# Kernel tuning notes

Hardware: AMD Instinct MI355X
Metric: run time of the kernel (lower is better)

The kernel has to match this reference:

```python
import jax, jax.numpy as jnp
import numpy as np

TOP_K = 2
HORIZON = 10


def _lstm_layer(seq, w_ih, w_hh, b_ih, b_hh):
    """Single torch-style LSTM layer over seq [T, in]; returns hidden seq [T, hid]."""
    hid = w_hh.shape[1]
    def step(carry, x_t):
        h, c = carry
        z = x_t @ w_ih.T + h @ w_hh.T + b_ih + b_hh  # [4*hid], torch gate order i,f,g,o
        i, f, g, o = jnp.split(z, 4)
        c = jax.nn.sigmoid(f) * c + jax.nn.sigmoid(i) * jnp.tanh(g)
        h = jax.nn.sigmoid(o) * jnp.tanh(c)
        return (h, c), h
    init = (jnp.zeros((hid,), seq.dtype), jnp.zeros((hid,), seq.dtype))
    _, hs = jax.lax.scan(step, init, seq)
    return hs


def setup_inputs() -> dict:
    key = jax.random.key(0)
    ks = jax.random.split(key, 12)
    H, E = 4096, 64
    B, S = 4, 4096
    s = 0.02
    return {
        "x": jax.random.normal(ks[0], (B, S, H), jnp.float32),
        "gate_w": jax.random.normal(ks[1], (E, H), jnp.float32) * s,
        "expert_bias": jnp.zeros((E,), jnp.float32),
        "cp_w1": jax.random.normal(ks[2], (64, H), jnp.float32) * s,
        "cp_b1": jnp.zeros((64,), jnp.float32),
        "cp_w2": jax.random.normal(ks[3], (1, 64), jnp.float32) * s,
        "cp_b2": jnp.zeros((1,), jnp.float32),
        "load_buffer": jax.random.uniform(ks[4], (50, E), jnp.float32),
        "lp_w_ih0": jax.random.normal(ks[5], (256, E), jnp.float32) * s,
        "lp_w_hh0": jax.random.normal(ks[6], (256, 64), jnp.float32) * s,
        "lp_b_ih0": jnp.zeros((256,), jnp.float32),
        "lp_b_hh0": jnp.zeros((256,), jnp.float32),
        "lp_w_ih1": jax.random.normal(ks[7], (256, 64), jnp.float32) * s,
        "lp_w_hh1": jax.random.normal(ks[8], (256, 64), jnp.float32) * s,
        "lp_b_ih1": jnp.zeros((256,), jnp.float32),
        "lp_b_hh1": jnp.zeros((256,), jnp.float32),
        "head_w": jax.random.normal(ks[9], (E * HORIZON, 64), jnp.float32) * s,
        "head_b": jnp.zeros((E * HORIZON,), jnp.float32),
    }


def reference(x, gate_w, expert_bias, cp_w1, cp_b1, cp_w2, cp_b2, load_buffer,
              lp_w_ih0, lp_w_hh0, lp_b_ih0, lp_b_hh0,
              lp_w_ih1, lp_w_hh1, lp_b_ih1, lp_b_hh1, head_w, head_b):
    sg = jax.lax.stop_gradient
    B, S, H = x.shape
    E = gate_w.shape[0]
    flat = x.reshape(-1, H)                       # [N, H]
    N = flat.shape[0]

    # --- routing logits (small gate GEMM) ---
    logits = flat @ gate_w.T                      # [N, E]

    # --- LSTM load prediction (torch.no_grad in original) ---
    seq = sg(load_buffer)
    h1 = _lstm_layer(seq, sg(lp_w_ih0), sg(lp_w_hh0), sg(lp_b_ih0), sg(lp_b_hh0))
    h2 = _lstm_layer(h1, sg(lp_w_ih1), sg(lp_w_hh1), sg(lp_b_ih1), sg(lp_b_hh1))
    pred = h2[-1] @ sg(head_w).T + sg(head_b)     # [E*HORIZON]
    future_load = jax.nn.softmax(pred.reshape(E, HORIZON).mean(axis=1))  # [E]

    # --- bias + predicted-load adjustment, softmax, top-k ---
    adj_logits = logits + expert_bias - sg(future_load)
    probs = jax.nn.softmax(adj_logits, axis=-1)   # [N, E]
    top_scores, top_idx = jax.lax.top_k(probs, TOP_K)
    top_scores = top_scores / top_scores.sum(axis=-1, keepdims=True)

    # --- switch-style load-balancing auxiliary loss ---
    one_hot = jax.nn.one_hot(top_idx, E, dtype=probs.dtype)   # [N, k, E]
    f = one_hot.sum(axis=(0, 1)) / (N * TOP_K)                # routed fraction per expert
    P = probs.mean(axis=0)                                    # mean routing prob
    aux_loss = E * jnp.sum(f * P)

    # --- dynamic capacity from complexity predictor (torch.no_grad) ---
    comp = jax.nn.sigmoid(
        jax.nn.relu(flat @ sg(cp_w1).T + sg(cp_b1)) @ sg(cp_w2).T + sg(cp_b2))  # [N,1]
    capacity = jnp.clip(0.5 + 1.5 * comp.mean(), 0.5, 2.0)

    return top_scores, top_idx, aux_loss, capacity, future_load
```

## Files before the change

### kernel.cpp

```cpp
#include <hip/hip_runtime.h>
#include <stdint.h>

#define IMG_OFF_BYTES 80000
#define CHUNK_IMG 16384
#define LOGITS_OFF 680000
#define TAU 1e-3f

#define XLOFF 5120
#define BUF_STRIDE 10240

typedef __attribute__((ext_vector_type(8))) short short8v;
typedef __attribute__((ext_vector_type(4))) short short4v;
typedef __attribute__((ext_vector_type(4))) float f32x4;

__device__ __forceinline__ float rlf(float v, int l) {
  return __int_as_float(__builtin_amdgcn_readlane(__float_as_int(v), l));
}
__device__ __forceinline__ float wsum(float v) {
#pragma unroll
  for (int o = 32; o; o >>= 1) v += __shfl_xor(v, o, 64);
  return v;
}
__device__ __forceinline__ float wmax(float v) {
#pragma unroll
  for (int o = 32; o; o >>= 1) v = fmaxf(v, __shfl_xor(v, o, 64));
  return v;
}
__device__ __forceinline__ unsigned short f2bf(float f) {
  unsigned u = __float_as_uint(f);
  u += 0x7fffu + ((u >> 16) & 1u);
  return (unsigned short)(u >> 16);
}
__device__ __forceinline__ float bf2f(unsigned short h) {
  return __uint_as_float(((unsigned)h) << 16);
}
__device__ __forceinline__ short8v frag8(const char* p0, const char* p1) {
  short4v a = *(const short4v*)p0;
  short4v b = *(const short4v*)p1;
  return __builtin_shufflevector(a, b, 0, 1, 2, 3, 4, 5, 6, 7);
}

__global__ __launch_bounds__(256) void prep_kernel(
    const float* __restrict__ gate_w, const float* __restrict__ cp_w1,
    float* __restrict__ ws)
{
  const int c = blockIdx.x;
  const int tid = threadIdx.x;
  if (c == 0 && tid < 144) ws[64 + tid] = 0.f;
  {
    float4 z = make_float4(0.f, 0.f, 0.f, 0.f);
    float4* lz = (float4*)(ws + LOGITS_OFF + c * 16384);
#pragma unroll
    for (int i = 0; i < 16; ++i) lz[tid + i * 256] = z;
  }
  const int row = tid >> 1;
  const int half = tid & 1;
  const float* src = ((row < 64) ? (gate_w + (size_t)row * 4096)
                                 : (cp_w1 + (size_t)(row - 64) * 4096)) + c * 32 + half * 16;
  float v[16];
#pragma unroll
  for (int j = 0; j < 4; ++j) *(float4*)&v[j * 4] = *(const float4*)(src + j * 4);
  const int g = row >> 4, r15 = row & 15;
  char* img = (char*)ws + IMG_OFF_BYTES + (size_t)c * CHUNK_IMG + g * 2048;
#pragma unroll
  for (int q = 0; q < 4; ++q) {
    unsigned short h0 = f2bf(v[4 * q + 0]), h1 = f2bf(v[4 * q + 1]);
    unsigned short h2 = f2bf(v[4 * q + 2]), h3 = f2bf(v[4 * q + 3]);
    unsigned short l0 = f2bf(v[4 * q + 0] - bf2f(h0));
    unsigned short l1 = f2bf(v[4 * q + 1] - bf2f(h1));
    unsigned short l2 = f2bf(v[4 * q + 2] - bf2f(h2));
    unsigned short l3 = f2bf(v[4 * q + 3] - bf2f(h3));
    uint2 hv, lv;
    hv.x = (unsigned)h0 | ((unsigned)h1 << 16);
    hv.y = (unsigned)h2 | ((unsigned)h3 << 16);
    lv.x = (unsigned)l0 | ((unsigned)l1 << 16);
    lv.y = (unsigned)l2 | ((unsigned)l3 << 16);
    const int l = q * 16 + r15;
    *(uint2*)(img + l * 16 + half * 8) = hv;
    *(uint2*)(img + 1024 + l * 16 + half * 8) = lv;
  }
}

__device__ void lstm_device(
    char* ldsbase,
    const float* __restrict__ lb,
    const float* __restrict__ wih0, const float* __restrict__ whh0,
    const float* __restrict__ bih0, const float* __restrict__ bhh0,
    const float* __restrict__ wih1, const float* __restrict__ whh1,
    const float* __restrict__ bih1, const float* __restrict__ bhh1,
    const float* __restrict__ head_w, const float* __restrict__ head_b,
    float* __restrict__ ws, float* __restrict__ out, int N)
{
  float* seqh = (float*)ldsbase;
  float* h1s  = seqh + 3200;
  float* zbuf = h1s + 3200;
  float* hbuf = zbuf + 256;
  float* preds = hbuf + 64;
  const int tid = threadIdx.x;
  const int lane = tid & 63;
  for (int i = tid; i < 3200; i += 256) seqh[i] = lb[i];

  float hv = 0.f;
#pragma unroll 1
  for (int L = 0; L < 2; ++L) {
    const float* wip  = L ? wih1 : wih0;
    const float* whp  = L ? whh1 : whh0;
    const float* bip  = L ? bih1 : bih0;
    const float* bhp  = L ? bhh1 : bhh0;
    const float* seqp = L ? h1s  : seqh;
    float wiR[64], whR[64];
#pragma unroll
    for (int j = 0; j < 64; j += 4) {
      *(float4*)&wiR[j] = *(const float4*)(wip + tid * 64 + j);
      *(float4*)&whR[j] = *(const float4*)(whp + tid * 64 + j);
    }
    const float bsum = bip[tid] + bhp[tid];
    float c_reg = 0.f;
    hv = 0.f;
    if (tid < 64) hbuf[tid] = 0.f;
    __syncthreads();
#pragma unroll 1
    for (int t = 0; t < 50; ++t) {
      const float xv = seqp[t * 64 + lane];
      float a0 = bsum, a1 = 0.f, a2 = 0.f, a3 = 0.f;
#pragma unroll
      for (int j = 0; j < 64; j += 4) {
        a0 = fmaf(rlf(xv, j + 0), wiR[j + 0], a0);
        a1 = fmaf(rlf(xv, j + 1), wiR[j + 1], a1);
        a2 = fmaf(rlf(xv, j + 2), wiR[j + 2], a2);
        a3 = fmaf(rlf(xv, j + 3), wiR[j + 3], a3);
      }
#pragma unroll
      for (int j = 0; j < 64; j += 4) {
        a0 = fmaf(rlf(hv, j + 0), whR[j + 0], a0);
        a1 = fmaf(rlf(hv, j + 1), whR[j + 1], a1);
        a2 = fmaf(rlf(hv, j + 2), whR[j + 2], a2);
        a3 = fmaf(rlf(hv, j + 3), whR[j + 3], a3);
      }
      zbuf[tid] = (a0 + a1) + (a2 + a3);
      __syncthreads();
      if (tid < 64) {
        const float zi = zbuf[tid], zf = zbuf[64 + tid];
        const float zg = zbuf[128 + tid], zo = zbuf[192 + tid];
        const float si = 1.f / (1.f + expf(-zi));
        const float sf = 1.f / (1.f + expf(-zf));
        const float so = 1.f / (1.f + expf(-zo));
        c_reg = sf * c_reg + si * tanhf(zg);
        const float h = so * tanhf(c_reg);
        hbuf[tid] = h;
        if (L == 0) h1s[t * 64 + tid] = h;
      }
      __syncthreads();
      hv = hbuf[lane];
    }
    __syncthreads();
  }
  for (int o = tid; o < 640; o += 256) {
    const float* hw = head_w + o * 64;
    float a0 = 0.f, a1 = 0.f, a2 = 0.f, a3 = 0.f;
#pragma unroll
    for (int j = 0; j < 64; j += 4) {
      a0 = fmaf(rlf(hv, j + 0), hw[j + 0], a0);
      a1 = fmaf(rlf(hv, j + 1), hw[j + 1], a1);
      a2 = fmaf(rlf(hv, j + 2), hw[j + 2], a2);
      a3 = fmaf(rlf(hv, j + 3), hw[j + 3], a3);
    }
    preds[o] = (a0 + a1) + (a2 + a3) + head_b[o];
  }
  __syncthreads();
  if (tid < 64) {
    float m = 0.f;
#pragma unroll
    for (int h = 0; h < 10; ++h) m += preds[tid * 10 + h];
    m = m / 10.f;
    const float mx = wmax(m);
    const float p = expf(m - mx);
    const float s = wsum(p);
    const float flv = p / s;
    ws[tid] = flv;
    out[4 * N + 2 + tid] = flv;
  }
}

__global__ __launch_bounds__(256, 1) void gemm_kernel(
    const float* __restrict__ x, float* __restrict__ ws, float* __restrict__ out,
    const float* __restrict__ lb,
    const float* __restrict__ wih0, const float* __restrict__ whh0,
    const float* __restrict__ bih0, const float* __restrict__ bhh0,
    const float* __restrict__ wih1, const float* __restrict__ whh1,
    const float* __restrict__ bih1, const float* __restrict__ bhh1,
    const float* __restrict__ head_w, const float* __restrict__ head_b,
    int N)
{
  __shared__ __align__(16) char lds[30720];
  if (blockIdx.x == 0) {
    lstm_device(lds, lb, wih0, whh0, bih0, bhh0, wih1, whh1, bih1, bhh1,
                head_w, head_b, ws, out, N);
    return;
  }
  const int b = blockIdx.x - 1;
  const int tb = (b & 255) * 64;
  const int ck0 = (b >> 8) * 32;
  const int tid = threadIdx.x;
  const int lane = tid & 63;
  const int wv = __builtin_amdgcn_readfirstlane(tid >> 6);
  const int r15 = lane & 15;
  const int fo = (lane >> 4) * 8;
  const int row = tid >> 2;
  const int kslot = tid & 3;
  const float* xsrc = x + (size_t)(tb + row) * 4096 + kslot * 8;
  const char* wimg = (const char*)ws + IMG_OFF_BYTES;
  char* buf0 = lds;
  char* buf1 = lds + BUF_STRIDE;

  f32x4 acc[4][2];
#pragma unroll
  for (int mi = 0; mi < 4; ++mi)
#pragma unroll
    for (int ni = 0; ni < 2; ++ni) acc[mi][ni] = (f32x4)0.f;

  float xa[8], xb[8];
  short8v wh[2], wl[2];

#define LOADX(R, C)                                                        \
  { *(float4*)&R[0] = *(const float4*)(xsrc + (size_t)(C) * 32);           \
    *(float4*)&R[4] = *(const float4*)(xsrc + (size_t)(C) * 32 + 4); }

#define WRITEX(R, BASE)                                                    \
  { uint4 hv, lv; unsigned hu[4], lu[4];                                   \
    _Pragma("unroll")                                                      \
    for (int i = 0; i < 4; ++i) {                                          \
      unsigned short h0 = f2bf(R[2 * i]), h1 = f2bf(R[2 * i + 1]);         \
      unsigned short l0 = f2bf(R[2 * i] - bf2f(h0));                       \
      unsigned short l1 = f2bf(R[2 * i + 1] - bf2f(h1));                   \
      hu[i] = (unsigned)h0 | ((unsigned)h1 << 16);                         \
      lu[i] = (unsigned)l0 | ((unsigned)l1 << 16);                         \
    }                                                                      \
    hv.x = hu[0]; hv.y = hu[1]; hv.z = hu[2]; hv.w = hu[3];                \
    lv.x = lu[0]; lv.y = lu[1]; lv.z = lu[2]; lv.w = lu[3];                \
    *(uint4*)((BASE) + row * 80 + kslot * 16) = hv;                        \
    *(uint4*)((BASE) + XLOFF + row * 80 + kslot * 16) = lv; }

#define WLOAD(C)                                                           \
  { const char* wb = wimg + (size_t)(C) * CHUNK_IMG + wv * 4096 + lane * 16; \
    wh[0] = *(const short8v*)wb;                                           \
    wl[0] = *(const short8v*)(wb + 1024);                                  \
    wh[1] = *(const short8v*)(wb + 2048);                                  \
    wl[1] = *(const short8v*)(wb + 3072); }

#define COMPUTE(BASE)                                                      \
  { short8v xh[4], xl[4];                                                  \
    _Pragma("unroll")                                                      \
    for (int mi = 0; mi < 4; ++mi) {                                       \
      const char* p = (BASE) + (mi * 16 + r15) * 80 + fo;                  \
      xh[mi] = frag8(p, p + 32);                                           \
      xl[mi] = frag8(p + XLOFF, p + XLOFF + 32);                           \
    }                                                                      \
    _Pragma("unroll")                                                      \
    for (int mi = 0; mi < 4; ++mi)                                         \
      _Pragma("unroll")                                                    \
      for (int ni = 0; ni < 2; ++ni) {                                     \
        acc[mi][ni] = __builtin_amdgcn_mfma_f32_16x16x32_bf16(             \
            xh[mi], wh[ni], acc[mi][ni], 0, 0, 0);                         \
        acc[mi][ni] = __builtin_amdgcn_mfma_f32_16x16x32_bf16(             \
            xh[mi], wl[ni], acc[mi][ni], 0, 0, 0);                         \
        acc[mi][ni] = __builtin_amdgcn_mfma_f32_16x16x32_bf16(             \
            xl[mi], wh[ni], acc[mi][ni], 0, 0, 0);                         \
      } }

  LOADX(xa, ck0);
  LOADX(xb, ck0 + 1);
  WRITEX(xa, buf0);
  __syncthreads();

#pragma unroll 1
  for (int cc = 0; cc < 16; ++cc) {
    const int c0 = ck0 + 2 * cc, c1 = c0 + 1;
    WLOAD(c0);
    if (cc < 15) LOADX(xa, c0 + 2);
    COMPUTE(buf0);
    WRITEX(xb, buf1);
    __syncthreads();
    WLOAD(c1);
    if (cc < 15) LOADX(xb, c1 + 2);
    COMPUTE(buf1);
    if (cc < 15) WRITEX(xa, buf0);
    __syncthreads();
  }

  float* lg = ws + LOGITS_OFF;
#pragma unroll
  for (int mi = 0; mi < 4; ++mi)
#pragma unroll
    for (int ni = 0; ni < 2; ++ni)
#pragma unroll
      for (int r = 0; r < 4; ++r) {
        const int tokrow = tb + mi * 16 + (lane >> 4) * 4 + r;
        const int col = wv * 32 + ni * 16 + r15;
        atomicAdd(&lg[(size_t)tokrow * 128 + col], acc[mi][ni][r]);
      }
#undef LOADX
#undef WRITEX
#undef WLOAD
#undef COMPUTE
}

__global__ __launch_bounds__(256) void epi_kernel(
    const float* __restrict__ eb_p, const float* __restrict__ cp_b1,
    const float* __restrict__ cp_w2, const float* __restrict__ cp_b2,
    float* __restrict__ ws, float* __restrict__ out, int N)
{
  const int tid = threadIdx.x;
  const int lane = tid & 63;
  const int wv = __builtin_amdgcn_readfirstlane(tid >> 6);
  const int tb = blockIdx.x * 32;
  const float* lg = ws + LOGITS_OFF;
  int* qd = (int*)(ws + 200);
  __shared__ float sP[64];
  __shared__ float scnt[64];
  __shared__ float scomp;
  if (tid < 64) { sP[tid] = 0.f; scnt[tid] = 0.f; }
  if (tid == 0) scomp = 0.f;
  __syncthreads();

  const float eb = eb_p[lane];
  const float fl = ws[lane];
  const float cb1 = cp_b1[lane];
  const float cw2 = cp_w2[lane];
  const float cb2 = cp_b2[0];
  float psum_local = 0.f, comp_local = 0.f;
  float* o_ts = out;
  float* o_ti = out + 2 * N;

#pragma unroll 1
  for (int tt = 0; tt < 8; ++tt) {
    const int tok = tb + wv * 8 + tt;
    const float lgv = lg[(size_t)tok * 128 + lane];
    const float lc  = lg[(size_t)tok * 128 + 64 + lane];
    float rr = fmaxf(lc + cb1, 0.f) * cw2;
    rr = wsum(rr);
    const float comp = 1.f / (1.f + expf(-(rr + cb2)));
    comp_local += comp;
    const float a = lgv + eb - fl;
    float m1 = a; int i1 = lane;
#pragma unroll
    for (int o = 32; o; o >>= 1) {
      const float ov = __shfl_xor(m1, o, 64);
      const int oi = __shfl_xor(i1, o, 64);
      if (ov > m1 || (ov == m1 && oi < i1)) { m1 = ov; i1 = oi; }
    }
    float m2 = (lane == i1) ? -1e30f : a; int i2 = lane;
#pragma unroll
    for (int o = 32; o; o >>= 1) {
      const float ov = __shfl_xor(m2, o, 64);
      const int oi = __shfl_xor(i2, o, 64);
      if (ov > m2 || (ov == m2 && oi < i2)) { m2 = ov; i2 = oi; }
    }
    float m3 = (lane == i1 || lane == i2) ? -1e30f : a;
#pragma unroll
    for (int o = 32; o; o >>= 1) m3 = fmaxf(m3, __shfl_xor(m3, o, 64));
    const float p = expf(a - m1);
    const float ssum = wsum(p);
    const float prob = p / ssum;
    psum_local += prob;
    const float s1 = rlf(prob, i1);
    const float s2 = rlf(prob, i2);
    if (lane == 0) {
      const float inv = 1.f / (s1 + s2);
      o_ts[tok * 2 + 0] = s1 * inv;
      o_ts[tok * 2 + 1] = s2 * inv;
      o_ti[tok * 2 + 0] = (float)i1;
      o_ti[tok * 2 + 1] = (float)i2;
      atomicAdd(&scnt[i1], 1.f);
      atomicAdd(&scnt[i2], 1.f);
      if (m1 - m2 < TAU || m2 - m3 < TAU) {
        int slot = atomicAdd(qd, 1);
        qd[8 + slot] = tok;
      }
    }
  }
  atomicAdd(&sP[lane], psum_local);
  if (lane == 0) atomicAdd(&scomp, comp_local);
  __syncthreads();
  if (tid < 64) {
    atomicAdd(&ws[64 + tid], sP[tid]);
    atomicAdd(&ws[128 + tid], scnt[tid]);
  }
  if (tid == 0) atomicAdd(&ws[192], scomp);
}

__global__ __launch_bounds__(256) void repair_kernel(
    const float* __restrict__ x, const float* __restrict__ gate_w,
    const float* __restrict__ eb_p, float* __restrict__ ws,
    float* __restrict__ out, int N)
{
  const int tid = threadIdx.x;
  __shared__ float red[256];
  int* qd = (int*)(ws + 200);
  const int qn = qd[0];
  float* o_ts = out;
  float* o_ti = out + 2 * N;

  for (int e = blockIdx.x; e < qn; e += gridDim.x) {
    const int tok = qd[8 + e];
    const int o = tid & 63;
    const int kq = tid >> 6;
    const float* xr = x + (size_t)tok * 4096 + kq * 1024;
    const float* wr = gate_w + (size_t)o * 4096 + kq * 1024;
    float s = 0.f;
#pragma unroll 4
    for (int j = 0; j < 256; ++j) {
      const float4 xv = *(const float4*)(xr + j * 4);
      const float4 wv = *(const float4*)(wr + j * 4);
      s = fmaf(xv.x, wv.x, s); s = fmaf(xv.y, wv.y, s);
      s = fmaf(xv.z, wv.z, s); s = fmaf(xv.w, wv.w, s);
    }
    red[tid] = s;
    __syncthreads();
    if (tid < 64) {
      const float a = red[tid] + red[64 + tid] + red[128 + tid] +
                      red[192 + tid] + eb_p[tid] - ws[tid];
      const int lane = tid;
      float m1 = a; int i1 = lane;
#pragma unroll
      for (int oo = 32; oo; oo >>= 1) {
        const float ov = __shfl_xor(m1, oo, 64);
        const int oi = __shfl_xor(i1, oo, 64);
        if (ov > m1 || (ov == m1 && oi < i1)) { m1 = ov; i1 = oi; }
      }
      float m2 = (lane == i1) ? -1e30f : a; int i2 = lane;
#pragma unroll
      for (int oo = 32; oo; oo >>= 1) {
        const float ov = __shfl_xor(m2, oo, 64);
        const int oi = __shfl_xor(i2, oo, 64);
        if (ov > m2 || (ov == m2 && oi < i2)) { m2 = ov; i2 = oi; }
      }
      const float p = expf(a - m1);
      const float ssum = wsum(p);
      const float s1 = rlf(p, i1) / ssum;
      const float s2 = rlf(p, i2) / ssum;
      if (lane == 0) {
        const int i1o = (int)o_ti[tok * 2 + 0];
        const int i2o = (int)o_ti[tok * 2 + 1];
        const float inv = 1.f / (s1 + s2);
        o_ts[tok * 2 + 0] = s1 * inv;
        o_ts[tok * 2 + 1] = s2 * inv;
        o_ti[tok * 2 + 0] = (float)i1;
        o_ti[tok * 2 + 1] = (float)i2;
        if (i1o != i1 || i2o != i2) {
          atomicAdd(&ws[128 + i1o], -1.f);
          atomicAdd(&ws[128 + i2o], -1.f);
          atomicAdd(&ws[128 + i1], 1.f);
          atomicAdd(&ws[128 + i2], 1.f);
        }
      }
    }
    __syncthreads();
  }
}

__global__ __launch_bounds__(64) void fin_kernel(const float* __restrict__ ws,
                                                 float* __restrict__ out, int N) {
  const int e = threadIdx.x;
  const float P = ws[64 + e] / (float)N;
  const float f = ws[128 + e] / (float)(2 * N);
  const float v = wsum(f * P);
  if (e == 0) {
    out[4 * N + 0] = 64.f * v;
    float cap = 0.5f + 1.5f * (ws[192] / (float)N);
    out[4 * N + 1] = fminf(fmaxf(cap, 0.5f), 2.f);
  }
}

extern "C" void kernel_launch(void* const* d_in, const int* in_sizes, int n_in,
                              void* d_out, int out_size, void* d_ws, size_t ws_size,
                              hipStream_t stream) {
  const float* x          = (const float*)d_in[0];
  const float* gate_w     = (const float*)d_in[1];
  const float* expert_bias= (const float*)d_in[2];
  const float* cp_w1      = (const float*)d_in[3];
  const float* cp_b1      = (const float*)d_in[4];
  const float* cp_w2      = (const float*)d_in[5];
  const float* cp_b2      = (const float*)d_in[6];
  const float* load_buffer= (const float*)d_in[7];
  const float* wih0       = (const float*)d_in[8];
  const float* whh0       = (const float*)d_in[9];
  const float* bih0       = (const float*)d_in[10];
  const float* bhh0       = (const float*)d_in[11];
  const float* wih1       = (const float*)d_in[12];
  const float* whh1       = (const float*)d_in[13];
  const float* bih1       = (const float*)d_in[14];
  const float* bhh1       = (const float*)d_in[15];
  const float* head_w     = (const float*)d_in[16];
  const float* head_b     = (const float*)d_in[17];
  float* out = (float*)d_out;
  float* ws  = (float*)d_ws;
  const int N = in_sizes[0] / 4096;

  prep_kernel<<<128, 256, 0, stream>>>(gate_w, cp_w1, ws);
  gemm_kernel<<<1025, 256, 0, stream>>>(x, ws, out, load_buffer,
                                        wih0, whh0, bih0, bhh0,
                                        wih1, whh1, bih1, bhh1,
                                        head_w, head_b, N);
  epi_kernel<<<N / 32, 256, 0, stream>>>(expert_bias, cp_b1, cp_w2, cp_b2,
                                         ws, out, N);
  repair_kernel<<<128, 256, 0, stream>>>(x, gate_w, expert_bias, ws, out, N);
  fin_kernel<<<1, 64, 0, stream>>>(ws, out, N);
}
```

Before: 196.4 us.

## Replace split-K atomic accumulation with per-split slabs reduced in epilogue

Measured after the change: 207.9 us. +5.9%, slower.

```diff
diff --git a/kernel.cpp b/kernel.cpp
--- a/kernel.cpp
+++ b/kernel.cpp
@@ -4,6 +4,7 @@
 #define IMG_OFF_BYTES 80000
 #define CHUNK_IMG 16384
 #define LOGITS_OFF 680000
+#define SLAB 2097152
 #define TAU 1e-3f
 
 #define XLOFF 5120
@@ -47,12 +48,6 @@
   const int c = blockIdx.x;
   const int tid = threadIdx.x;
   if (c == 0 && tid < 144) ws[64 + tid] = 0.f;
-  {
-    float4 z = make_float4(0.f, 0.f, 0.f, 0.f);
-    float4* lz = (float4*)(ws + LOGITS_OFF + c * 16384);
-#pragma unroll
-    for (int i = 0; i < 16; ++i) lz[tid + i * 256] = z;
-  }
   const int row = tid >> 1;
   const int half = tid & 1;
   const float* src = ((row < 64) ? (gate_w + (size_t)row * 4096)
@@ -192,7 +187,7 @@
     const float* __restrict__ head_w, const float* __restrict__ head_b,
     int N)
 {
-  __shared__ __align__(16) char lds[30720];
+  __shared__ __align__(16) char lds[34048];
   if (blockIdx.x == 0) {
     lstm_device(lds, lb, wih0, whh0, bih0, bhh0, wih1, whh1, bih1, bhh1,
                 head_w, head_b, ws, out, N);
@@ -200,7 +195,8 @@
   }
   const int b = blockIdx.x - 1;
   const int tb = (b & 255) * 64;
-  const int ck0 = (b >> 8) * 32;
+  const int kq = b >> 8;
+  const int ck0 = kq * 32;
   const int tid = threadIdx.x;
   const int lane = tid & 63;
   const int wv = __builtin_amdgcn_readfirstlane(tid >> 6);
@@ -288,17 +284,24 @@
     __syncthreads();
   }
 
-  float* lg = ws + LOGITS_OFF;
+  float (*souts)[132] = (float(*)[132])lds;
 #pragma unroll
   for (int mi = 0; mi < 4; ++mi)
 #pragma unroll
     for (int ni = 0; ni < 2; ++ni)
 #pragma unroll
-      for (int r = 0; r < 4; ++r) {
-        const int tokrow = tb + mi * 16 + (lane >> 4) * 4 + r;
-        const int col = wv * 32 + ni * 16 + r15;
-        atomicAdd(&lg[(size_t)tokrow * 128 + col], acc[mi][ni][r]);
-      }
+      for (int r = 0; r < 4; ++r)
+        souts[mi * 16 + (lane >> 4) * 4 + r][wv * 32 + ni * 16 + r15] =
+            acc[mi][ni][r];
+  __syncthreads();
+  {
+    float* slab = ws + LOGITS_OFF + (size_t)kq * SLAB;
+    const int srow = tid >> 2, sq = tid & 3;
+    float4* dst = (float4*)(slab + (size_t)(tb + srow) * 128 + sq * 32);
+    const float4* srcp = (const float4*)&souts[srow][sq * 32];
+#pragma unroll
+    for (int i = 0; i < 8; ++i) dst[i] = srcp[i];
+  }
 #undef LOADX
 #undef WRITEX
 #undef WLOAD
@@ -335,8 +338,11 @@
 #pragma unroll 1
   for (int tt = 0; tt < 8; ++tt) {
     const int tok = tb + wv * 8 + tt;
-    const float lgv = lg[(size_t)tok * 128 + lane];
-    const float lc  = lg[(size_t)tok * 128 + 64 + lane];
+    const size_t base = (size_t)tok * 128;
+    const float lgv = ((lg[base + lane] + lg[SLAB + base + lane]) +
+                       (lg[2 * SLAB + base + lane] + lg[3 * SLAB + base + lane]));
+    const float lc  = ((lg[base + 64 + lane] + lg[SLAB + base + 64 + lane]) +
+                       (lg[2 * SLAB + base + 64 + lane] + lg[3 * SLAB + base + 64 + lane]));
     float rr = fmaxf(lc + cb1, 0.f) * cw2;
     rr = wsum(rr);
     const float comp = 1.f / (1.f + expf(-(rr + cb2)));
```
